# Kernel tuning notes

Hardware: AMD Instinct MI355X
Metric: run time of the kernel (lower is better)

## Reference

```python
import jax, jax.numpy as jnp
import numpy as np

B, T, C = 8, 2048, 1024
N_HEAD = 16
HEAD_DIM = C // N_HEAD  # 64


def setup_inputs() -> dict:
    key = jax.random.key(0)
    k1, k2, k3 = jax.random.split(key, 3)
    x = jax.random.normal(k1, (B, T, C), dtype=jnp.float32)
    # qkv projection: Linear(C, 3*head_dim) with bias
    W = jax.random.normal(k2, (C, 3 * HEAD_DIM), dtype=jnp.float32) * (1.0 / np.sqrt(C))
    b = jax.random.normal(k3, (3 * HEAD_DIM,), dtype=jnp.float32) * 0.01
    return {"x": x, "W": W, "b": b}


def reference(x, W, b):
    # qkv projection, then chunk into (k, q, v) -- note key comes first in the original
    kqv = x @ W + b                       # [B, T, 3*hd]
    k, q, v = jnp.split(kqv, 3, axis=-1)  # each [B, T, hd]
    scale = HEAD_DIM ** -0.5
    wei = jnp.einsum('bth,bsh->bts', q, k) * scale  # [B, T, T]
    t = x.shape[1]
    causal = jnp.tril(jnp.ones((t, t), dtype=bool))
    wei = jnp.where(causal, wei, -jnp.inf)
    wei = jax.nn.softmax(wei, axis=-1)
    # dropout p=0.0 -> identity
    out = jnp.einsum('bts,bsh->bth', wei, v)  # [B, T, hd]
    return out
```

## Files before the change

### kernel.cpp

```cpp
#include <hip/hip_runtime.h>

#define NB 8
#define NT 2048
#define NC 1024
#define HD 64
#define N3 192

typedef float f32x4 __attribute__((ext_vector_type(4)));
typedef _Float16 f16x8 __attribute__((ext_vector_type(8)));
typedef short short8 __attribute__((ext_vector_type(8)));
typedef short short4v __attribute__((ext_vector_type(4)));

static __device__ __forceinline__ short f2h(float f) {
  _Float16 h = (_Float16)f;
  return __builtin_bit_cast(short, h);
}
static __device__ __forceinline__ unsigned pk2h(float a, float b) {
  unsigned lo = (unsigned short)f2h(a);
  unsigned hi = (unsigned short)f2h(b);
  return lo | (hi << 16);
}

typedef __attribute__((address_space(1))) const void* gptr1;
typedef __attribute__((address_space(3))) void* sptr3;
static __device__ __forceinline__ void gload_lds16(const void* g, void* s) {
  __builtin_amdgcn_global_load_lds((gptr1)g, (sptr3)s, 16, 0, 0);
}

__launch_bounds__(256)
__global__ void prep_w(const float* __restrict__ W, short* __restrict__ Wt,
                       float* __restrict__ kmax2) {
  if (blockIdx.x == 0 && threadIdx.x < 8) kmax2[threadIdx.x] = 0.f;
  const int n = threadIdx.x;
  if (n >= 192) return;
  const int k0 = blockIdx.x * 16;
  short8 v0, v1;
#pragma unroll
  for (int j = 0; j < 8; ++j) v0[j] = f2h(W[(size_t)(k0 + j) * N3 + n]);
#pragma unroll
  for (int j = 0; j < 8; ++j) v1[j] = f2h(W[(size_t)(k0 + 8 + j) * N3 + n]);
  *(short8*)(Wt + (size_t)n * NC + k0) = v0;
  *(short8*)(Wt + (size_t)n * NC + k0 + 8) = v1;
}

__launch_bounds__(256, 2)
__global__ void qkv_proj(const float* __restrict__ x, const short* __restrict__ Wt,
                         const float* __restrict__ bias, short* __restrict__ Kb,
                         short* __restrict__ Qb, short* __restrict__ Vt,
                         float* __restrict__ kmax2) {
  __shared__ short Ax[2][32 * 64];
  __shared__ short Bw[2][192 * 64];

  const int tid = threadIdx.x;
  const int lane = tid & 63;
  const int wave = tid >> 6;
  const int wr = wave >> 1, wc = wave & 1;
  const int r0 = blockIdx.x * 32;
  const int batch = r0 >> 11;
  const int t0 = r0 & (NT - 1);
  const int g = lane >> 4, c = lane & 15;

  const int bsub = lane >> 3;
  const size_t bgoff = (size_t)bsub * (NC * 2) + (size_t)((lane & 7) ^ bsub) * 16;

  f32x4 acc[6];
#pragma unroll
  for (int nt = 0; nt < 6; ++nt) acc[nt] = (f32x4){0.f, 0.f, 0.f, 0.f};

  float4 areg[2];

  auto stage_B = [&](int kt, int p) {
    const char* src = (const char*)Wt + (size_t)(wave * 48) * (NC * 2) +
                      (size_t)kt * 128 + bgoff;
    char* dst = (char*)Bw[p] + wave * 48 * 128;
#pragma unroll
    for (int j = 0; j < 6; ++j)
      gload_lds16(src + (size_t)(j * 8) * (NC * 2), dst + j * 8 * 128);
  };
  auto load_A = [&](int kt) {
    const float* xp = x + (size_t)r0 * NC + kt * 64;
#pragma unroll
    for (int i = 0; i < 2; ++i) {
      int idx = tid + 256 * i;
      int row = idx >> 4, c4 = idx & 15;
      areg[i] = *(const float4*)(xp + (size_t)row * NC + c4 * 4);
    }
  };
  auto write_A = [&](int p) {
#pragma unroll
    for (int i = 0; i < 2; ++i) {
      int idx = tid + 256 * i;
      int row = idx >> 4, c4 = idx & 15;
      int byte = row * 128 + ((c4 * 8) ^ ((row & 7) << 4));
      float4 v = areg[i];
      short4v h;
      h[0] = f2h(v.x); h[1] = f2h(v.y); h[2] = f2h(v.z); h[3] = f2h(v.w);
      *(short4v*)((char*)Ax[p] + byte) = h;
    }
  };
  auto compute = [&](int p) {
#pragma unroll
    for (int kc = 0; kc < 2; ++kc) {
      const int arow = wr * 16 + c;
      f16x8 a = *(const f16x8*)((const char*)Ax[p] + arow * 128 +
                                ((kc * 64 + (g << 4)) ^ ((arow & 7) << 4)));
#pragma unroll
      for (int nt = 0; nt < 6; ++nt) {
        const int brow = wc * 96 + nt * 16 + c;
        f16x8 b = *(const f16x8*)((const char*)Bw[p] + brow * 128 +
                                  ((kc * 64 + (g << 4)) ^ ((brow & 7) << 4)));
        acc[nt] = __builtin_amdgcn_mfma_f32_16x16x32_f16(a, b, acc[nt], 0, 0, 0);
      }
    }
  };

  stage_B(0, 0);
  load_A(0);
  write_A(0);
  __syncthreads();
#pragma unroll 1
  for (int kt = 0; kt < 16; ++kt) {
    const int p = kt & 1;
    if (kt < 15) { stage_B(kt + 1, p ^ 1); load_A(kt + 1); }
    compute(p);
    if (kt < 15) write_A(p ^ 1);
    __syncthreads();
  }

  float bv[6];
#pragma unroll
  for (int nt = 0; nt < 6; ++nt) bv[nt] = bias[wc * 96 + nt * 16 + c];

  short* VTl = (short*)Ax[0];
  float knorm[4] = {0.f, 0.f, 0.f, 0.f};
#pragma unroll
  for (int nt = 0; nt < 6; ++nt) {
#pragma unroll
    for (int i = 0; i < 4; ++i) {
      int n = wc * 96 + nt * 16 + c;
      int lrow = wr * 16 + (g << 2) + i;
      float v = acc[nt][i] + bv[nt];
      size_t tok = ((size_t)batch << 11) | (size_t)(t0 + lrow);
      if (n < 64) {
        Kb[tok * HD + n] = f2h(v);
        knorm[i] += v * v;
      } else if (n < 128) {
        Qb[tok * HD + (n - 64)] = f2h(v);
      } else {
        int h = n - 128;
        int byte = h * 64 + ((lrow * 2) ^ ((h & 3) << 4));
        *(short*)((char*)VTl + byte) = f2h(v);
      }
    }
  }
  if (wc == 0) {
#pragma unroll
    for (int d = 1; d < 16; d <<= 1)
#pragma unroll
      for (int i = 0; i < 4; ++i) knorm[i] += __shfl_xor(knorm[i], d);
    float mx = fmaxf(fmaxf(knorm[0], knorm[1]), fmaxf(knorm[2], knorm[3]));
    if (c == 0) atomicMax((int*)(kmax2 + batch), __float_as_int(mx));
  }
  __syncthreads();
  {
    int h = tid >> 2, ch = tid & 3;
    short8 v = *(const short8*)((const char*)VTl + h * 64 +
                                ((ch * 16) ^ ((h & 3) << 4)));
    *(short8*)(Vt + (((size_t)(batch * HD + h)) << 11) + (size_t)t0 + ch * 8) = v;
  }
}

#define PPITCH 136
__launch_bounds__(256)
__global__ void attn(const short* __restrict__ Kb, const short* __restrict__ Qb,
                     const short* __restrict__ Vt, const float* __restrict__ kmax2,
                     float* __restrict__ out) {
  __shared__ char Pl[4][16 * PPITCH];

  const int tid = threadIdx.x, lane = tid & 63, wave = tid >> 6;
  const int g = lane >> 4, c = lane & 15;
  const int qt = blockIdx.x & 31;
  const int b = blockIdx.x >> 5;
  const int nkv = qt + 1;
  const int q0 = qt * 64;
  const int qg = q0 + wave * 16 + c;
  const float c2 = 0.125f * 1.44269504088896340736f;

  f16x8 qa[2];
  {
    size_t base = ((size_t)b * NT + (size_t)qg) * HD + (g << 3);
    qa[0] = *(const f16x8*)(Qb + base);
    qa[1] = *(const f16x8*)(Qb + base + 32);
  }
  float m2;
  {
    float qn = 0.f;
#pragma unroll
    for (int kc = 0; kc < 2; ++kc)
#pragma unroll
      for (int j = 0; j < 8; ++j) {
        float qv = (float)qa[kc][j];
        qn += qv * qv;
      }
    qn += __shfl_xor(qn, 16);
    qn += __shfl_xor(qn, 32);
    m2 = sqrtf(qn) * sqrtf(kmax2[b]) * c2;
  }

  f32x4 o[4];
#pragma unroll
  for (int nt = 0; nt < 4; ++nt) o[nt] = (f32x4){0.f, 0.f, 0.f, 0.f};
  float l_r = 0.f;

  const short* kbp = Kb + ((size_t)b * NT) * HD;
  const short* vbp = Vt + (((size_t)b * HD) << 11);
  char* pw = Pl[wave];

  f16x8 kA[4][2], vA[4][2], kB[4][2], vB[4][2];

  auto loadKV = [&](f16x8 (&kf)[4][2], f16x8 (&vf)[4][2], int t) {
    const int s0 = t * 64;
#pragma unroll
    for (int st = 0; st < 4; ++st) {
      size_t rb = (size_t)(s0 + st * 16 + c) * HD + (g << 3);
      kf[st][0] = *(const f16x8*)(kbp + rb);
      kf[st][1] = *(const f16x8*)(kbp + rb + 32);
      size_t vb = (((size_t)(st * 16 + c)) << 11) + (size_t)s0 + (g << 3);
      vf[st][0] = *(const f16x8*)(vbp + vb);
      vf[st][1] = *(const f16x8*)(vbp + vb + 32);
    }
  };

  auto step = [&](f16x8 (&kf)[4][2], f16x8 (&vf)[4][2], int t) {
    const int s0 = t * 64;
    f32x4 s[4];
#pragma unroll
    for (int st = 0; st < 4; ++st) s[st] = (f32x4){0.f, 0.f, 0.f, 0.f};
#pragma unroll
    for (int kc = 0; kc < 2; ++kc)
#pragma unroll
      for (int st = 0; st < 4; ++st)
        s[st] = __builtin_amdgcn_mfma_f32_16x16x32_f16(kf[st][kc], qa[kc], s[st], 0, 0, 0);

    const bool diag = (t == qt);
#pragma unroll
    for (int st = 0; st < 4; ++st) {
      float pv[4];
#pragma unroll
      for (int i = 0; i < 4; ++i) {
        int sg = s0 + st * 16 + (g << 2) + i;
        float p = __builtin_amdgcn_exp2f(s[st][i] * c2 - m2);
        pv[i] = (diag && sg > qg) ? 0.f : p;
      }
      l_r += (pv[0] + pv[1]) + (pv[2] + pv[3]);
      uint2 w;
      w.x = pk2h(pv[0], pv[1]);
      w.y = pk2h(pv[2], pv[3]);
      *(uint2*)(pw + c * PPITCH + st * 32 + g * 8) = w;
    }

#pragma unroll
    for (int kc = 0; kc < 2; ++kc) {
      uint2 h0 = *(const uint2*)(pw + c * PPITCH + kc * 64 + g * 16);
      uint2 h1 = *(const uint2*)(pw + c * PPITCH + kc * 64 + g * 16 + 8);
      f16x8 pa;
      *(uint2*)&pa = h0;
      *((uint2*)&pa + 1) = h1;
#pragma unroll
      for (int nt = 0; nt < 4; ++nt)
        o[nt] = __builtin_amdgcn_mfma_f32_16x16x32_f16(pa, vf[nt][kc], o[nt], 0, 0, 0);
    }
  };

  loadKV(kA, vA, 0);
  int t = 0;
  while (true) {
    if (t + 1 < nkv) loadKV(kB, vB, t + 1);
    step(kA, vA, t);
    ++t;
    if (t >= nkv) break;
    if (t + 1 < nkv) loadKV(kA, vA, t + 1);
    step(kB, vB, t);
    ++t;
    if (t >= nkv) break;
  }

  l_r += __shfl_xor(l_r, 16);
  l_r += __shfl_xor(l_r, 32);
  float* outb = out + ((size_t)b * NT + (size_t)(q0 + wave * 16)) * HD;
#pragma unroll
  for (int i = 0; i < 4; ++i) {
    int r = (g << 2) + i;
    float inv = 1.0f / __shfl(l_r, r);
#pragma unroll
    for (int nt = 0; nt < 4; ++nt)
      outb[(size_t)r * HD + nt * 16 + c] = o[nt][i] * inv;
  }
}

extern "C" void kernel_launch(void* const* d_in, const int* in_sizes, int n_in,
                              void* d_out, int out_size, void* d_ws, size_t ws_size,
                              hipStream_t stream) {
  const float* x = (const float*)d_in[0];
  const float* W = (const float*)d_in[1];
  const float* bias = (const float*)d_in[2];
  float* out = (float*)d_out;

  char* ws = (char*)d_ws;
  float* kmax2 = (float*)ws;
  short* Wt = (short*)(ws + 2048);
  short* Kb = Wt + (size_t)N3 * NC;
  short* Qb = Kb + (size_t)NB * NT * HD;
  short* Vt = Qb + (size_t)NB * NT * HD;

  prep_w<<<64, 256, 0, stream>>>(W, Wt, kmax2);
  qkv_proj<<<512, 256, 0, stream>>>(x, Wt, bias, Kb, Qb, Vt, kmax2);
  attn<<<NB * 32, 256, 0, stream>>>(Kb, Qb, Vt, kmax2, out);
}
```

Measured before the change: 173.1 us.

## Stage K/V tiles through swizzled LDS with async global-to-LDS double buffering

Replaces per-wave register loads of K and V tiles with cooperative direct global-to-LDS loads shared by all four waves, double-buffered and swizzled to avoid bank conflicts. Each wave previously fetched the full K/V tile itself, so the block now does a quarter of the global traffic for K/V. The block index mapping is also changed so batches interleave across consecutive blocks. In exchange it adds a block-wide barrier per KV tile, LDS reads before each MFMA, and extra LDS usage that may lower occupancy.

After: 151.5 us. 12.5% less time.

```diff
diff --git a/kernel.cpp b/kernel.cpp
--- a/kernel.cpp
+++ b/kernel.cpp
@@ -175,12 +175,14 @@
 __global__ void attn(const short* __restrict__ Kb, const short* __restrict__ Qb,
                      const short* __restrict__ Vt, const float* __restrict__ kmax2,
                      float* __restrict__ out) {
+  __shared__ char Kld[2][64 * 128];
+  __shared__ char Vld[2][64 * 128];
   __shared__ char Pl[4][16 * PPITCH];
 
   const int tid = threadIdx.x, lane = tid & 63, wave = tid >> 6;
   const int g = lane >> 4, c = lane & 15;
-  const int qt = blockIdx.x & 31;
-  const int b = blockIdx.x >> 5;
+  const int b = blockIdx.x & 7;
+  const int qt = blockIdx.x >> 3;
   const int nkv = qt + 1;
   const int q0 = qt * 64;
   const int qg = q0 + wave * 16 + c;
@@ -212,35 +214,42 @@
   for (int nt = 0; nt < 4; ++nt) o[nt] = (f32x4){0.f, 0.f, 0.f, 0.f};
   float l_r = 0.f;
 
-  const short* kbp = Kb + ((size_t)b * NT) * HD;
-  const short* vbp = Vt + (((size_t)b * HD) << 11);
+  const int sub = lane >> 3, chx = (lane & 7) ^ sub;
+  const char* ksrc = (const char*)Kb + ((size_t)b * NT) * 128;
+  const char* vsrc = (const char*)Vt + ((size_t)b * HD) * 4096;
   char* pw = Pl[wave];
 
-  f16x8 kA[4][2], vA[4][2], kB[4][2], vB[4][2];
-
-  auto loadKV = [&](f16x8 (&kf)[4][2], f16x8 (&vf)[4][2], int t) {
+  auto STAGE = [&](int t, int p) {
     const int s0 = t * 64;
-#pragma unroll
-    for (int st = 0; st < 4; ++st) {
-      size_t rb = (size_t)(s0 + st * 16 + c) * HD + (g << 3);
-      kf[st][0] = *(const f16x8*)(kbp + rb);
-      kf[st][1] = *(const f16x8*)(kbp + rb + 32);
-      size_t vb = (((size_t)(st * 16 + c)) << 11) + (size_t)s0 + (g << 3);
-      vf[st][0] = *(const f16x8*)(vbp + vb);
-      vf[st][1] = *(const f16x8*)(vbp + vb + 32);
-    }
-  };
-
-  auto step = [&](f16x8 (&kf)[4][2], f16x8 (&vf)[4][2], int t) {
+    const char* kp = ksrc + (size_t)(s0 + wave * 16 + sub) * 128 + (size_t)chx * 16;
+    const char* vp = vsrc + (size_t)(wave * 16 + sub) * 4096 + (size_t)s0 * 2 +
+                     (size_t)chx * 16;
+    gload_lds16(kp, Kld[p] + (wave * 16) * 128);
+    gload_lds16(kp + 8 * 128, Kld[p] + (wave * 16 + 8) * 128);
+    gload_lds16(vp, Vld[p] + (wave * 16) * 128);
+    gload_lds16(vp + (size_t)8 * 4096, Vld[p] + (wave * 16 + 8) * 128);
+  };
+
+  STAGE(0, 0);
+  __syncthreads();
+  int cur = 0;
+#pragma unroll 1
+  for (int t = 0; t < nkv; ++t) {
+    if (t + 1 < nkv) STAGE(t + 1, cur ^ 1);
     const int s0 = t * 64;
+
     f32x4 s[4];
 #pragma unroll
     for (int st = 0; st < 4; ++st) s[st] = (f32x4){0.f, 0.f, 0.f, 0.f};
 #pragma unroll
     for (int kc = 0; kc < 2; ++kc)
 #pragma unroll
-      for (int st = 0; st < 4; ++st)
-        s[st] = __builtin_amdgcn_mfma_f32_16x16x32_f16(kf[st][kc], qa[kc], s[st], 0, 0, 0);
+      for (int st = 0; st < 4; ++st) {
+        const int krow = st * 16 + c;
+        f16x8 kf = *(const f16x8*)(Kld[cur] + krow * 128 +
+                                   ((kc * 64 + (g << 4)) ^ ((krow & 7) << 4)));
+        s[st] = __builtin_amdgcn_mfma_f32_16x16x32_f16(kf, qa[kc], s[st], 0, 0, 0);
+      }
 
     const bool diag = (t == qt);
 #pragma unroll
@@ -267,22 +276,15 @@
       *(uint2*)&pa = h0;
       *((uint2*)&pa + 1) = h1;
 #pragma unroll
-      for (int nt = 0; nt < 4; ++nt)
-        o[nt] = __builtin_amdgcn_mfma_f32_16x16x32_f16(pa, vf[nt][kc], o[nt], 0, 0, 0);
-    }
-  };
-
-  loadKV(kA, vA, 0);
-  int t = 0;
-  while (true) {
-    if (t + 1 < nkv) loadKV(kB, vB, t + 1);
-    step(kA, vA, t);
-    ++t;
-    if (t >= nkv) break;
-    if (t + 1 < nkv) loadKV(kA, vA, t + 1);
-    step(kB, vB, t);
-    ++t;
-    if (t >= nkv) break;
+      for (int nt = 0; nt < 4; ++nt) {
+        const int vrow = nt * 16 + c;
+        f16x8 vv = *(const f16x8*)(Vld[cur] + vrow * 128 +
+                                   ((kc * 64 + (g << 4)) ^ ((vrow & 7) << 4)));
+        o[nt] = __builtin_amdgcn_mfma_f32_16x16x32_f16(pa, vv, o[nt], 0, 0, 0);
+      }
+    }
+    __syncthreads();
+    cur ^= 1;
   }
 
   l_r += __shfl_xor(l_r, 16);
```
